# Performance work log

Measured on AMD Instinct MI355X. Metric: run time of the kernel, lower is better.

The kernel has to match this reference:

```python
import jax, jax.numpy as jnp
import numpy as np

N = 4096      # nodes (= attention seq_len)
D = 256       # dim_h
H = 4         # num_heads
HD = D // H   # head dim
E = 131072    # edges (avg degree 32)


def _ln(x, g, b, eps=1e-5):
    mu = jnp.mean(x, -1, keepdims=True)
    var = jnp.var(x, -1, keepdims=True)
    return (x - mu) * jax.lax.rsqrt(var + eps) * g + b


def setup_inputs() -> dict:
    key = jax.random.key(0)
    ks = jax.random.split(key, 10)
    s = 0.02
    nrm = lambda k, shape: jax.random.normal(k, shape, jnp.float32) * s
    return dict(
        x=jax.random.normal(ks[0], (N, D), jnp.float32),
        edge_index=jax.random.randint(ks[1], (2, E), 0, N, dtype=jnp.int32),
        W_gcn=nrm(ks[2], (D, D)), b_gcn=jnp.zeros((D,), jnp.float32),
        w_qkv=nrm(ks[3], (D, 3 * D)), b_qkv=jnp.zeros((3 * D,), jnp.float32),
        w_out=nrm(ks[4], (D, D)), b_out=jnp.zeros((D,), jnp.float32),
        g1l=jnp.ones((D,), jnp.float32), beta1l=jnp.zeros((D,), jnp.float32),
        g1a=jnp.ones((D,), jnp.float32), beta1a=jnp.zeros((D,), jnp.float32),
        W1=nrm(ks[5], (D, 2 * D)), bf1=jnp.zeros((2 * D,), jnp.float32),
        W2=nrm(ks[6], (2 * D, D)), bf2=jnp.zeros((D,), jnp.float32),
        g2=jnp.ones((D,), jnp.float32), beta2=jnp.zeros((D,), jnp.float32),
    )


def reference(x, edge_index, W_gcn, b_gcn, w_qkv, b_qkv, w_out, b_out,
              g1l, beta1l, g1a, beta1a, W1, bf1, W2, bf2, g2, beta2):
    n = x.shape[0]
    # --- GCNConv: sym-normalized aggregation with self loops ---
    loop = jnp.arange(n, dtype=edge_index.dtype)
    src = jnp.concatenate([edge_index[0], loop])
    dst = jnp.concatenate([edge_index[1], loop])
    deg = jax.ops.segment_sum(jnp.ones_like(src, x.dtype), dst, num_segments=n)
    dinv = jax.lax.rsqrt(deg)  # deg >= 1 thanks to self loops
    h = x @ W_gcn                                  # [N, D]
    msg = h[src] * (dinv[src] * dinv[dst])[:, None]  # gather + edge norm
    x_local = jax.ops.segment_sum(msg, dst, num_segments=n) + b_gcn
    x = _ln(x + x_local, g1l, beta1l)
    # --- Multi-head self-attention over all nodes (one sequence) ---
    qkv = x @ w_qkv + b_qkv
    q, k, v = jnp.split(qkv, 3, axis=-1)
    q = q.reshape(n, H, HD)
    k = k.reshape(n, H, HD)
    v = v.reshape(n, H, HD)
    scale = 1.0 / (HD ** 0.5)
    scores = jnp.einsum('nhd,mhd->hnm', q, k) * scale   # [H, N, N]
    attn = jax.nn.softmax(scores, axis=-1)
    x_attn = jnp.einsum('hnm,mhd->nhd', attn, v).reshape(n, D) @ w_out + b_out
    x = _ln(x + x_attn, g1a, beta1a)
    # --- FFN (D -> 2D -> D, ReLU) ---
    x_ffn = jax.nn.relu(x @ W1 + bf1) @ W2 + bf2
    return _ln(x + x_ffn, g2, beta2)
```

## Files before the change

### kernel.cpp

```cpp
#include <hip/hip_runtime.h>

typedef unsigned short u16;
typedef __bf16 bf16x8 __attribute__((ext_vector_type(8)));
typedef float f32x4 __attribute__((ext_vector_type(4)));
typedef float f32x16 __attribute__((ext_vector_type(16)));
typedef unsigned u32x4v __attribute__((ext_vector_type(4)));

__device__ __forceinline__ u16 f2u(float f) {
    unsigned u = __builtin_bit_cast(unsigned, f);
    return (u16)((u + 0x7FFFu + ((u >> 16) & 1u)) >> 16);
}

__device__ __forceinline__ float u2f(u16 h) {
    return __builtin_bit_cast(float, (unsigned)h << 16);
}

__device__ __forceinline__ void glds16(const u16* g, u16* l) {
    __builtin_amdgcn_global_load_lds((const __attribute__((address_space(1))) unsigned int*)g,
                                     (__attribute__((address_space(3))) unsigned int*)l, 16, 0, 0);
}


__global__ __launch_bounds__(256) void prep_k(
    const float* __restrict__ w0, const float* __restrict__ w1, const float* __restrict__ w2,
    const float* __restrict__ w3, const float* __restrict__ w4, const float* __restrict__ x,
    u16* __restrict__ o0, u16* __restrict__ o1, u16* __restrict__ o2,
    u16* __restrict__ o3, u16* __restrict__ o4, u16* __restrict__ xo,
    int* __restrict__ cnt, int xblocks, int nn) {
    int b = blockIdx.x, t = threadIdx.x;
    if (b < 144) {
        const float* in; u16* out; int R, C, tb;
        if (b < 16)       { in = w0; out = o0; R = 256; C = 256; tb = b; }
        else if (b < 64)  { in = w1; out = o1; R = 256; C = 768; tb = b - 16; }
        else if (b < 80)  { in = w2; out = o2; R = 256; C = 256; tb = b - 64; }
        else if (b < 112) { in = w3; out = o3; R = 256; C = 512; tb = b - 80; }
        else              { in = w4; out = o4; R = 512; C = 256; tb = b - 112; }
        int tcols = C >> 6;
        int tr = tb / tcols, tc = tb - tr * tcols;
        __shared__ float T[64][65];
        int i0 = t >> 6, j = t & 63;
#pragma unroll
        for (int p = 0; p < 16; p++) {
            int r = p * 4 + i0;
            T[r][j] = in[(long)(tr * 64 + r) * C + tc * 64 + j];
        }
        __syncthreads();
#pragma unroll
        for (int p = 0; p < 16; p++) {
            int c = p * 4 + i0;
            out[(long)(tc * 64 + c) * R + tr * 64 + j] = f2u(T[j][c]);
        }
    } else if (b < 144 + xblocks) {
        long base = (long)(b - 144) * 4096;
#pragma unroll
        for (int p = 0; p < 4; p++) {
            long idx = base + p * 1024 + t * 4;
            float4 v = *(const float4*)&x[idx];
            unsigned lo = (unsigned)f2u(v.x) | ((unsigned)f2u(v.y) << 16);
            unsigned hi = (unsigned)f2u(v.z) | ((unsigned)f2u(v.w) << 16);
            *(uint2*)&xo[idx] = uint2{lo, hi};
        }
    } else {
        int i = (b - 144 - xblocks) * 256 + t;
        if (i < nn) cnt[i] = 0;
    }
}


__device__ __forceinline__ void block_ln_stats(float v, float& mu, float& rstd) {
    float s1 = v, s2 = v * v;
#pragma unroll
    for (int m = 1; m < 64; m <<= 1) { s1 += __shfl_xor(s1, m, 64); s2 += __shfl_xor(s2, m, 64); }
    __shared__ float r1[4], r2[4];
    int lane = threadIdx.x & 63, w = threadIdx.x >> 6;
    if (lane == 0) { r1[w] = s1; r2[w] = s2; }
    __syncthreads();
    s1 = r1[0] + r1[1] + r1[2] + r1[3];
    s2 = r2[0] + r2[1] + r2[2] + r2[3];
    mu = s1 * (1.0f / 256.0f);
    float var = s2 * (1.0f / 256.0f) - mu * mu;
    rstd = rsqrtf(var + 1e-5f);
}


__global__ __launch_bounds__(256) void gcn_agg_ln_k(
    const u16* __restrict__ h, const float* __restrict__ x,
    const int* __restrict__ srcs, const int* __restrict__ cnt,
    const float* __restrict__ bg,
    const float* __restrict__ g, const float* __restrict__ be,
    float* __restrict__ x1, u16* __restrict__ x1bf) {
    int n = blockIdx.x, d = threadIdx.x;
    int c = cnt[n]; c = c < 128 ? c : 128;
    int st = n << 7;
    float dn = rsqrtf((float)(c + 1));
    float agg = u2f(h[(long)n * 256 + d]) * dn;
    int e = 0;
    for (; e + 4 <= c; e += 4) {
        int s0 = srcs[st + e], s1 = srcs[st + e + 1], s2 = srcs[st + e + 2], s3 = srcs[st + e + 3];
        float a0 = u2f(h[(long)s0 * 256 + d]) * rsqrtf((float)(cnt[s0] + 1));
        float a1 = u2f(h[(long)s1 * 256 + d]) * rsqrtf((float)(cnt[s1] + 1));
        float a2 = u2f(h[(long)s2 * 256 + d]) * rsqrtf((float)(cnt[s2] + 1));
        float a3 = u2f(h[(long)s3 * 256 + d]) * rsqrtf((float)(cnt[s3] + 1));
        agg += (a0 + a1) + (a2 + a3);
    }
    for (; e < c; e++) {
        int s = srcs[st + e];
        agg += u2f(h[(long)s * 256 + d]) * rsqrtf((float)(cnt[s] + 1));
    }
    float v = x[(long)n * 256 + d] + dn * agg + bg[d];
    float mu, rs;
    block_ln_stats(v, mu, rs);
    float y = (v - mu) * rs * g[d] + be[d];
    x1[(long)n * 256 + d] = y;
    x1bf[(long)n * 256 + d] = f2u(y);
}


template <int EPI>
__device__ __forceinline__ void gemm_body(
    int bx, int by,
    const u16* __restrict__ A, const u16* __restrict__ Bt,
    const float* __restrict__ bias, void* __restrict__ outp,
    int M, int N, int K) {
    __shared__ __align__(16) u16 As[64 * 128];
    __shared__ __align__(16) u16 Bs[64 * 128];
    int tid = threadIdx.x;
    int lane = tid & 63, w = tid >> 6;
    int l15 = lane & 15, quad = lane >> 4, l7 = l15 & 7;
    int m0 = bx * 64, n0 = by * 64;
    int wm = (w >> 1) * 32, wn = (w & 1) * 32;
    f32x4 acc[2][2];
#pragma unroll
    for (int i = 0; i < 2; i++)
#pragma unroll
        for (int j = 0; j < 2; j++) acc[i][j] = f32x4{0.f, 0.f, 0.f, 0.f};

    int rA0 = (wm + l15) * 128, rA1 = (wm + 16 + l15) * 128;
    int rB0 = (wn + l15) * 128, rB1 = (wn + 16 + l15) * 128;

    for (int kb = 0; kb < K; kb += 128) {
        if (kb) __syncthreads();
#pragma unroll
        for (int i = 0; i < 4; i++) {
            int s = i * 256 + tid;
            int j = s >> 4, dch = s & 15;
            int c = dch ^ (j & 7);
            glds16(A + (long)(m0 + j) * K + kb + c * 8, &As[s * 8]);
            glds16(Bt + (long)(n0 + j) * K + kb + c * 8, &Bs[s * 8]);
        }
        __syncthreads();
#pragma unroll
        for (int step = 0; step < 4; step++) {
            int d8 = (((step << 2) + quad) ^ l7) << 3;
            bf16x8 af0 = *(const bf16x8*)&As[rA0 + d8];
            bf16x8 af1 = *(const bf16x8*)&As[rA1 + d8];
            bf16x8 bf0 = *(const bf16x8*)&Bs[rB0 + d8];
            bf16x8 bf1 = *(const bf16x8*)&Bs[rB1 + d8];
            acc[0][0] = __builtin_amdgcn_mfma_f32_16x16x32_bf16(af0, bf0, acc[0][0], 0, 0, 0);
            acc[0][1] = __builtin_amdgcn_mfma_f32_16x16x32_bf16(af0, bf1, acc[0][1], 0, 0, 0);
            acc[1][0] = __builtin_amdgcn_mfma_f32_16x16x32_bf16(af1, bf0, acc[1][0], 0, 0, 0);
            acc[1][1] = __builtin_amdgcn_mfma_f32_16x16x32_bf16(af1, bf1, acc[1][1], 0, 0, 0);
        }
    }

#pragma unroll
    for (int nf = 0; nf < 2; nf++) {
        int col = n0 + wn + nf * 16 + l15;
        float bv = bias ? bias[col] : 0.0f;
#pragma unroll
        for (int mf = 0; mf < 2; mf++) {
#pragma unroll
            for (int r = 0; r < 4; r++) {
                int row = m0 + wm + mf * 16 + quad * 4 + r;
                float v = acc[mf][nf][r] + bv;
                if (EPI == 1) {
                    u16* q = (u16*)outp;
                    u16* kk = q + (long)M * 256;
                    u16* vt = kk + (long)M * 256;
                    if (col < 256) {
                        q[(((col >> 6) * (long)M) + row) * 64 + (col & 63)] = f2u(v * 0.180336884f);
                    } else if (col < 512) {
                        int c = col - 256;
                        kk[(((c >> 6) * (long)M) + row) * 64 + (c & 63)] = f2u(v);
                    } else {
                        int c = col - 512;
                        vt[((c >> 6) * 64 + (c & 63)) * (long)M + row] = f2u(v);
                    }
                } else {
                    ((u16*)outp)[(long)row * N + col] = f2u(v);
                }
            }
        }
    }
}

template <int EPI>
__global__ __launch_bounds__(256) void gemm_k(
    const u16* __restrict__ A, const u16* __restrict__ Bt,
    const float* __restrict__ bias, void* __restrict__ outp,
    int M, int N, int K) {
    gemm_body<EPI>(blockIdx.x, blockIdx.y, A, Bt, bias, outp, M, N, K);
}


template <int WRITE_BF>
__global__ __launch_bounds__(512) void gemm_ln_k(
    const u16* __restrict__ A, const u16* __restrict__ Bt, const float* __restrict__ bias,
    const float* __restrict__ res, const float* __restrict__ g, const float* __restrict__ be,
    float* __restrict__ outf, u16* __restrict__ outbf, int M, int K) {
    __shared__ __align__(16) u16 As[16 * 64];
    __shared__ __align__(16) u16 Bs[256 * 64];
    __shared__ float red[2][8][16];
    int tid = threadIdx.x;
    int lane = tid & 63, w = tid >> 6;
    int l15 = lane & 15, quad = lane >> 4, l7 = l15 & 7;
    int m0 = blockIdx.x * 16;
    f32x4 acc[2];
#pragma unroll
    for (int i = 0; i < 2; i++) acc[i] = f32x4{0.f, 0.f, 0.f, 0.f};

    int jA = tid >> 3, dA = tid & 7, cA = dA ^ (jA & 7);
    const u16* agp = A + (long)(m0 + jA) * K + cA * 8;

    for (int kb = 0; kb < K; kb += 64) {
        if (kb) __syncthreads();
        if (tid < 128) glds16(agp + kb, &As[tid * 8]);
#pragma unroll
        for (int i = 0; i < 4; i++) {
            int s = i * 512 + tid;
            int jb = s >> 3, db = s & 7, cb = db ^ (jb & 7);
            glds16(Bt + (long)jb * K + kb + cb * 8, &Bs[s * 8]);
        }
        __syncthreads();
#pragma unroll
        for (int step = 0; step < 2; step++) {
            int d8 = (((step << 2) + quad) ^ l7) << 3;
            bf16x8 af = *(const bf16x8*)&As[l15 * 64 + d8];
#pragma unroll
            for (int nf = 0; nf < 2; nf++) {
                int rb = w * 32 + nf * 16 + l15;
                bf16x8 bfr = *(const bf16x8*)&Bs[rb * 64 + d8];
                acc[nf] = __builtin_amdgcn_mfma_f32_16x16x32_bf16(af, bfr, acc[nf], 0, 0, 0);
            }
        }
    }

    float vv[2][4];
    float p1[4] = {0.f, 0.f, 0.f, 0.f}, p2[4] = {0.f, 0.f, 0.f, 0.f};
#pragma unroll
    for (int nf = 0; nf < 2; nf++) {
        int col = w * 32 + nf * 16 + l15;
        float bv = bias[col];
#pragma unroll
        for (int r = 0; r < 4; r++) {
            int row = m0 + quad * 4 + r;
            float v = acc[nf][r] + bv + res[(long)row * 256 + col];
            vv[nf][r] = v;
            p1[r] += v; p2[r] += v * v;
        }
    }
#pragma unroll
    for (int m = 1; m < 16; m <<= 1) {
#pragma unroll
        for (int r = 0; r < 4; r++) {
            p1[r] += __shfl_xor(p1[r], m, 64);
            p2[r] += __shfl_xor(p2[r], m, 64);
        }
    }
    if (l15 == 0) {
#pragma unroll
        for (int r = 0; r < 4; r++) { red[0][w][quad * 4 + r] = p1[r]; red[1][w][quad * 4 + r] = p2[r]; }
    }
    __syncthreads();
    float mu[4], rs[4];
#pragma unroll
    for (int r = 0; r < 4; r++) {
        int rr = quad * 4 + r;
        float s1 = 0.f, s2 = 0.f;
#pragma unroll
        for (int ww = 0; ww < 8; ww++) { s1 += red[0][ww][rr]; s2 += red[1][ww][rr]; }
        mu[r] = s1 * (1.0f / 256.0f);
        float var = s2 * (1.0f / 256.0f) - mu[r] * mu[r];
        rs[r] = rsqrtf(var + 1e-5f);
    }
#pragma unroll
    for (int nf = 0; nf < 2; nf++) {
        int col = w * 32 + nf * 16 + l15;
        float gg = g[col], bb = be[col];
#pragma unroll
        for (int r = 0; r < 4; r++) {
            int row = m0 + quad * 4 + r;
            float y = (vv[nf][r] - mu[r]) * rs[r] * gg + bb;
            outf[(long)row * 256 + col] = y;
            if (WRITE_BF) outbf[(long)row * 256 + col] = f2u(y);
        }
    }
}


__global__ __launch_bounds__(512) void ffn_fused_k(
    const u16* __restrict__ A, const u16* __restrict__ W1t, const float* __restrict__ b1,
    const u16* __restrict__ W2t, const float* __restrict__ b2v,
    const float* __restrict__ res, const float* __restrict__ g, const float* __restrict__ be,
    float* __restrict__ outf, int M) {
    __shared__ __align__(16) u16 As[16 * 64];
    __shared__ __align__(16) u16 Bs[256 * 64];
    __shared__ __align__(16) u16 Hs[16 * 512];
    __shared__ float red[2][8][16];
    int tid = threadIdx.x;
    int lane = tid & 63, w = tid >> 6;
    int l15 = lane & 15, quad = lane >> 4, l7 = l15 & 7;
    int m0 = blockIdx.x * 16;

    int jA = tid >> 3, dA = tid & 7, cA = dA ^ (jA & 7);
    const u16* agp = A + (long)(m0 + jA) * 256 + cA * 8;

#pragma unroll
    for (int hf = 0; hf < 2; hf++) {
        f32x4 acc[2];
#pragma unroll
        for (int i = 0; i < 2; i++) acc[i] = f32x4{0.f, 0.f, 0.f, 0.f};
        for (int kb = 0; kb < 256; kb += 64) {
            if (hf | kb) __syncthreads();
            if (tid < 128) glds16(agp + kb, &As[tid * 8]);
#pragma unroll
            for (int i = 0; i < 4; i++) {
                int s = i * 512 + tid;
                int jb = s >> 3, db = s & 7, cb = db ^ (jb & 7);
                glds16(W1t + (long)(hf * 256 + jb) * 256 + kb + cb * 8, &Bs[s * 8]);
            }
            __syncthreads();
#pragma unroll
            for (int step = 0; step < 2; step++) {
                int d8 = (((step << 2) + quad) ^ l7) << 3;
                bf16x8 af = *(const bf16x8*)&As[l15 * 64 + d8];
#pragma unroll
                for (int nf = 0; nf < 2; nf++) {
                    int rb = w * 32 + nf * 16 + l15;
                    bf16x8 bfr = *(const bf16x8*)&Bs[rb * 64 + d8];
                    acc[nf] = __builtin_amdgcn_mfma_f32_16x16x32_bf16(af, bfr, acc[nf], 0, 0, 0);
                }
            }
        }
#pragma unroll
        for (int nf = 0; nf < 2; nf++) {
            int col = hf * 256 + w * 32 + nf * 16 + l15;
            float bv = b1[col];
            int g8 = col >> 3, e = col & 7;
#pragma unroll
            for (int r = 0; r < 4; r++) {
                int row = quad * 4 + r;
                float v = acc[nf][r] + bv;
                int slot = (g8 & ~7) | ((g8 & 7) ^ (row & 7));
                Hs[row * 512 + slot * 8 + e] = f2u(v > 0.f ? v : 0.f);
            }
        }
    }

    f32x4 acc[2];
#pragma unroll
    for (int i = 0; i < 2; i++) acc[i] = f32x4{0.f, 0.f, 0.f, 0.f};
    for (int kb = 0; kb < 512; kb += 64) {
        __syncthreads();
#pragma unroll
        for (int i = 0; i < 4; i++) {
            int s = i * 512 + tid;
            int jb = s >> 3, db = s & 7, cb = db ^ (jb & 7);
            glds16(W2t + (long)jb * 512 + kb + cb * 8, &Bs[s * 8]);
        }
        __syncthreads();
#pragma unroll
        for (int step = 0; step < 2; step++) {
            int d8 = (((step << 2) + quad) ^ l7) << 3;
            bf16x8 af = *(const bf16x8*)&Hs[l15 * 512 + kb + d8];
#pragma unroll
            for (int nf = 0; nf < 2; nf++) {
                int rb = w * 32 + nf * 16 + l15;
                bf16x8 bfr = *(const bf16x8*)&Bs[rb * 64 + d8];
                acc[nf] = __builtin_amdgcn_mfma_f32_16x16x32_bf16(af, bfr, acc[nf], 0, 0, 0);
            }
        }
    }

    float vv[2][4];
    float p1[4] = {0.f, 0.f, 0.f, 0.f}, p2[4] = {0.f, 0.f, 0.f, 0.f};
#pragma unroll
    for (int nf = 0; nf < 2; nf++) {
        int col = w * 32 + nf * 16 + l15;
        float bv = b2v[col];
#pragma unroll
        for (int r = 0; r < 4; r++) {
            int row = m0 + quad * 4 + r;
            float v = acc[nf][r] + bv + res[(long)row * 256 + col];
            vv[nf][r] = v;
            p1[r] += v; p2[r] += v * v;
        }
    }
#pragma unroll
    for (int m = 1; m < 16; m <<= 1) {
#pragma unroll
        for (int r = 0; r < 4; r++) {
            p1[r] += __shfl_xor(p1[r], m, 64);
            p2[r] += __shfl_xor(p2[r], m, 64);
        }
    }
    if (l15 == 0) {
#pragma unroll
        for (int r = 0; r < 4; r++) { red[0][w][quad * 4 + r] = p1[r]; red[1][w][quad * 4 + r] = p2[r]; }
    }
    __syncthreads();
    float mu[4], rs[4];
#pragma unroll
    for (int r = 0; r < 4; r++) {
        int rr = quad * 4 + r;
        float s1 = 0.f, s2 = 0.f;
#pragma unroll
        for (int ww = 0; ww < 8; ww++) { s1 += red[0][ww][rr]; s2 += red[1][ww][rr]; }
        mu[r] = s1 * (1.0f / 256.0f);
        float var = s2 * (1.0f / 256.0f) - mu[r] * mu[r];
        rs[r] = rsqrtf(var + 1e-5f);
    }
#pragma unroll
    for (int nf = 0; nf < 2; nf++) {
        int col = w * 32 + nf * 16 + l15;
        float gg = g[col], bb = be[col];
#pragma unroll
        for (int r = 0; r < 4; r++) {
            int row = m0 + quad * 4 + r;
            outf[(long)row * 256 + col] = (vv[nf][r] - mu[r]) * rs[r] * gg + bb;
        }
    }
}


__global__ __launch_bounds__(256) void front_k(
    const int* __restrict__ ei, int E, int* __restrict__ cnt, int* __restrict__ srcs,
    const u16* __restrict__ A, const u16* __restrict__ Bt, void* __restrict__ outp,
    int M, int N, int K, int SB) {
    int b = blockIdx.x;
    if (b < SB) {
        int e = b * 256 + threadIdx.x;
        if (e < E) {
            int s = ei[e], d = ei[E + e];
            int p = atomicAdd(&cnt[d], 1);
            if (p < 128) srcs[(d << 7) + p] = s;
        }
    } else {
        int id = b - SB;
        gemm_body<3>(id & 63, id >> 6, A, Bt, nullptr, outp, M, N, K);
    }
}


__global__ __launch_bounds__(256) void attn_k(const u16* __restrict__ qg, const u16* __restrict__ kg,
                                              const u16* __restrict__ vtg, u16* __restrict__ po,
                                              float* __restrict__ pl, int N, int S) {
    int tid = threadIdx.x;
    int w = tid >> 6, lane = tid & 63;
    int l31 = lane & 31, h = lane >> 5, xr = l31 & 7;
    int qb = blockIdx.x, hh = blockIdx.y, sp = blockIdx.z;
    int q0w = qb * 128 + w * 32;
    int kbeg = sp * (N / S);
    int nit = (N / S) / 64;
    const u16* qh = qg + (long)hh * N * 64;
    const u16* kh = kg + (long)hh * N * 64;
    const u16* vh = vtg + (long)hh * 64 * N;

    __shared__ __align__(16) u16 KV[2][2][4096];

    int s0 = tid, j0 = s0 >> 3, c0s = ((s0 & 7) ^ (j0 & 7)) * 8;
    int s1 = tid + 256, j1 = s1 >> 3, c1s = ((s1 & 7) ^ (j1 & 7)) * 8;
    const u16* kp0 = kh + (long)(kbeg + j0) * 64 + c0s;
    const u16* kp1 = kh + (long)(kbeg + j1) * 64 + c1s;
    const u16* vp0 = vh + (long)j0 * N + kbeg + c0s;
    const u16* vp1 = vh + (long)j1 * N + kbeg + c1s;
    u16* lk0[2] = {&KV[0][0][s0 * 8], &KV[1][0][s0 * 8]};
    u16* lk1[2] = {&KV[0][0][s1 * 8], &KV[1][0][s1 * 8]};
    u16* lv0[2] = {&KV[0][1][s0 * 8], &KV[1][1][s0 * 8]};
    u16* lv1[2] = {&KV[0][1][s1 * 8], &KV[1][1][s1 * 8]};

    bf16x8 qf[4];
#pragma unroll
    for (int stp = 0; stp < 4; stp++)
        qf[stp] = *(const bf16x8*)(qh + (long)(q0w + l31) * 64 + stp * 16 + h * 8);

    f32x16 o0{}, o1{};
    float ll = 0.f;

    glds16(kp0, lk0[0]); glds16(kp1, lk1[0]);
    glds16(vp0, lv0[0]); glds16(vp1, lv1[0]);
    kp0 += 4096; kp1 += 4096; vp0 += 64; vp1 += 64;

    for (int it = 0; it < nit; it++) {
        __syncthreads();
        if (it + 1 < nit) {
            int nb = (it + 1) & 1;
            glds16(kp0, lk0[nb]); glds16(kp1, lk1[nb]);
            glds16(vp0, lv0[nb]); glds16(vp1, lv1[nb]);
            kp0 += 4096; kp1 += 4096; vp0 += 64; vp1 += 64;
        }
        const u16* Kc = &KV[it & 1][0][0];
        const u16* Vc = &KV[it & 1][1][0];

        f32x16 sA{}, sB{};
#pragma unroll
        for (int stp = 0; stp < 4; stp++) {
            int cc = (((stp << 1) + h) ^ xr) * 8;
            bf16x8 kfa = *(const bf16x8*)&Kc[l31 * 64 + cc];
            bf16x8 kfb = *(const bf16x8*)&Kc[(32 + l31) * 64 + cc];
            sA = __builtin_amdgcn_mfma_f32_32x32x16_bf16(kfa, qf[stp], sA, 0, 0, 0);
            sB = __builtin_amdgcn_mfma_f32_32x32x16_bf16(kfb, qf[stp], sB, 0, 0, 0);
        }

#pragma unroll
        for (int kt = 0; kt < 2; kt++) {
            f32x16 s = kt ? sB : sA;
            unsigned wr[8];
#pragma unroll
            for (int i = 0; i < 8; i++) {
                unsigned ua = (unsigned)((int)(s[2 * i] * 8388608.0f) + 1064992209);
                unsigned ub = (unsigned)((int)(s[2 * i + 1] * 8388608.0f) + 1064992209);
                ll += __builtin_bit_cast(float, ua & 0xffff0000u);
                ll += __builtin_bit_cast(float, ub & 0xffff0000u);
                wr[i] = __builtin_amdgcn_perm(ub, ua, 0x07060302u);
            }
            asm("v_permlane32_swap_b32 %0, %1" : "+v"(wr[2]), "+v"(wr[0]));
            asm("v_permlane32_swap_b32 %0, %1" : "+v"(wr[3]), "+v"(wr[1]));
            asm("v_permlane32_swap_b32 %0, %1" : "+v"(wr[6]), "+v"(wr[4]));
            asm("v_permlane32_swap_b32 %0, %1" : "+v"(wr[7]), "+v"(wr[5]));
            u32x4v t0 = {wr[0], wr[1], wr[2], wr[3]};
            u32x4v t1 = {wr[4], wr[5], wr[6], wr[7]};
            bf16x8 f0 = __builtin_bit_cast(bf16x8, t0);
            bf16x8 f1 = __builtin_bit_cast(bf16x8, t1);

#pragma unroll
            for (int dt = 0; dt < 2; dt++) {
                int rowb = (dt * 32 + l31) * 64;
                bf16x8 v0 = *(const bf16x8*)&Vc[rowb + (((kt << 2) + h) ^ xr) * 8];
                bf16x8 v1 = *(const bf16x8*)&Vc[rowb + (((kt << 2) + 2 + h) ^ xr) * 8];
                if (dt == 0) {
                    o0 = __builtin_amdgcn_mfma_f32_32x32x16_bf16(f0, v0, o0, 0, 0, 0);
                    o0 = __builtin_amdgcn_mfma_f32_32x32x16_bf16(f1, v1, o0, 0, 0, 0);
                } else {
                    o1 = __builtin_amdgcn_mfma_f32_32x32x16_bf16(f0, v0, o1, 0, 0, 0);
                    o1 = __builtin_amdgcn_mfma_f32_32x32x16_bf16(f1, v1, o1, 0, 0, 0);
                }
            }
        }
    }

    ll += __shfl_xor(ll, 32, 64);
    long pbase = ((long)(sp * 4 + hh)) * N;
#pragma unroll
    for (int dt = 0; dt < 2; dt++)
#pragma unroll
        for (int r = 0; r < 16; r++) {
            int qrow = q0w + (r & 3) + ((r >> 2) << 3) + (h << 2);
            float val = dt ? o1[r] : o0[r];
            po[(pbase + qrow) * 64 + dt * 32 + l31] = f2u(val);
        }
    if (lane < 32) pl[pbase + q0w + lane] = ll;
}

__global__ __launch_bounds__(256) void attn_comb_k(const u16* __restrict__ po, const float* __restrict__ pl,
                                                   u16* __restrict__ xo, int N, int S) {
    int n = blockIdx.x, c = threadIdx.x;
    int hh = c >> 6, d = c & 63;
    float osum = 0.f, lsum = 0.f;
    for (int s = 0; s < S; s++) {
        osum += u2f(po[(((long)(s * 4 + hh)) * N + n) * 64 + d]);
        lsum += pl[((long)(s * 4 + hh)) * N + n];
    }
    xo[(long)n * 256 + c] = f2u(osum / lsum);
}


extern "C" void kernel_launch(void* const* d_in, const int* in_sizes, int n_in,
                              void* d_out, int out_size, void* d_ws, size_t ws_size,
                              hipStream_t stream) {
    const float* x    = (const float*)d_in[0];
    const int*   ei   = (const int*)d_in[1];
    const float* Wg   = (const float*)d_in[2];
    const float* bg   = (const float*)d_in[3];
    const float* Wqkv = (const float*)d_in[4];
    const float* bqkv = (const float*)d_in[5];
    const float* Wo   = (const float*)d_in[6];
    const float* bo   = (const float*)d_in[7];
    const float* g1l  = (const float*)d_in[8];
    const float* b1l  = (const float*)d_in[9];
    const float* g1a  = (const float*)d_in[10];
    const float* b1a  = (const float*)d_in[11];
    const float* W1   = (const float*)d_in[12];
    const float* bf1  = (const float*)d_in[13];
    const float* W2   = (const float*)d_in[14];
    const float* bf2  = (const float*)d_in[15];
    const float* g2   = (const float*)d_in[16];
    const float* b2   = (const float*)d_in[17];
    float* out = (float*)d_out;

    int N = in_sizes[0] / 256;
    int E = in_sizes[1] / 2;
    const int S = 8;

    char* p = (char*)d_ws;
    auto alloc = [&](size_t bytes) { void* r = (void*)p; p += (bytes + 255) & ~(size_t)255; return r; };
    u16*   wg_t   = (u16*)alloc((size_t)256 * 256 * 2);
    u16*   wqkv_t = (u16*)alloc((size_t)256 * 768 * 2);
    u16*   wo_t   = (u16*)alloc((size_t)256 * 256 * 2);
    u16*   w1_t   = (u16*)alloc((size_t)512 * 256 * 2);
    u16*   w2_t   = (u16*)alloc((size_t)256 * 512 * 2);
    u16*   xbf    = (u16*)alloc((size_t)N * 256 * 2);
    u16*   h      = (u16*)alloc((size_t)N * 256 * 2);
    int*   cnt    = (int*)alloc((size_t)N * 4);
    int*   srcs   = (int*)alloc((size_t)N * 128 * 4);
    float* x1     = (float*)alloc((size_t)N * 256 * 4);
    u16*   x1bf   = (u16*)alloc((size_t)N * 256 * 2);
    u16*   qkv    = (u16*)alloc((size_t)3 * N * 256 * 2);
    u16*   xattn  = (u16*)alloc((size_t)N * 256 * 2);
    float* x2     = (float*)alloc((size_t)N * 256 * 4);
    u16*   x2bf   = (u16*)alloc((size_t)N * 256 * 2);
    u16*   po     = (u16*)alloc((size_t)S * 4 * N * 64 * 2);
    float* pl     = (float*)alloc((size_t)S * 4 * N * 4);

    dim3 b256(256);

    int xblocks = (N * 256) / 4096;
    int cblocks = (N + 255) / 256;
    prep_k<<<144 + xblocks + cblocks, b256, 0, stream>>>(Wg, Wqkv, Wo, W1, W2, x,
                                                         wg_t, wqkv_t, wo_t, w1_t, w2_t, xbf,
                                                         cnt, xblocks, N);

    int SB = (E + 255) / 256;
    front_k<<<SB + (N / 64) * 4, b256, 0, stream>>>(ei, E, cnt, srcs, xbf, wg_t, h, N, 256, 256, SB);

    gcn_agg_ln_k<<<N, b256, 0, stream>>>(h, x, srcs, cnt, bg, g1l, b1l, x1, x1bf);

    gemm_k<1><<<dim3(N / 64, 12), b256, 0, stream>>>(x1bf, wqkv_t, bqkv, qkv, N, 768, 256);

    attn_k<<<dim3(N / 128, 4, S), b256, 0, stream>>>(qkv, qkv + (size_t)N * 256, qkv + (size_t)2 * N * 256,
                                                     po, pl, N, S);
    attn_comb_k<<<N, b256, 0, stream>>>(po, pl, xattn, N, S);

    gemm_ln_k<1><<<N / 16, dim3(512), 0, stream>>>(xattn, wo_t, bo, x1, g1a, b1a, x2, x2bf, N, 256);

    ffn_fused_k<<<N / 16, dim3(512), 0, stream>>>(x2bf, w1_t, bf1, w2_t, bf2, x2, g2, b2, out, N);
}
```

Baseline: 189.0 us.

## Accumulate split-KV attention partials with atomics and fuse combine into out-proj GEMM

Attention splits now atomicAdd their fp32 partial outputs and row sums into one zeroed N×256 buffer instead of writing per-split bf16 partials. The separate combine kernel is removed, and the output-projection GEMM+LN kernel does the normalisation (po/pl) while staging A into LDS. This cuts a launch and the S-fold partial-buffer traffic. In exchange it adds zeroing work in prep, fp32 atomic contention across the 8 splits, and nondeterministic summation order.

```diff
diff --git a/kernel.cpp b/kernel.cpp
--- a/kernel.cpp
+++ b/kernel.cpp
@@ -26,7 +26,7 @@
     const float* __restrict__ w3, const float* __restrict__ w4, const float* __restrict__ x,
     u16* __restrict__ o0, u16* __restrict__ o1, u16* __restrict__ o2,
     u16* __restrict__ o3, u16* __restrict__ o4, u16* __restrict__ xo,
-    int* __restrict__ cnt, int xblocks, int nn) {
+    float* __restrict__ pz, int* __restrict__ cnt, int xblocks, int zblocks, int nn) {
     int b = blockIdx.x, t = threadIdx.x;
     if (b < 144) {
         const float* in; u16* out; int R, C, tb;
@@ -60,8 +60,15 @@
             unsigned hi = (unsigned)f2u(v.z) | ((unsigned)f2u(v.w) << 16);
             *(uint2*)&xo[idx] = uint2{lo, hi};
         }
+    } else if (b < 144 + xblocks + zblocks) {
+        long base = (long)(b - 144 - xblocks) * 4096;
+#pragma unroll
+        for (int p = 0; p < 4; p++) {
+            long idx = base + p * 1024 + t * 4;
+            *(float4*)&pz[idx] = float4{0.f, 0.f, 0.f, 0.f};
+        }
     } else {
-        int i = (b - 144 - xblocks) * 256 + t;
+        int i = (b - 144 - xblocks - zblocks) * 256 + t;
         if (i < nn) cnt[i] = 0;
     }
 }
@@ -203,39 +210,55 @@
 }
 
 
-template <int WRITE_BF>
-__global__ __launch_bounds__(512) void gemm_ln_k(
-    const u16* __restrict__ A, const u16* __restrict__ Bt, const float* __restrict__ bias,
+__global__ __launch_bounds__(512) void comb_gemm_ln_k(
+    const float* __restrict__ po, const float* __restrict__ pl,
+    const u16* __restrict__ Bt, const float* __restrict__ bias,
     const float* __restrict__ res, const float* __restrict__ g, const float* __restrict__ be,
-    float* __restrict__ outf, u16* __restrict__ outbf, int M, int K) {
-    __shared__ __align__(16) u16 As[16 * 64];
+    float* __restrict__ outf, u16* __restrict__ outbf, int M) {
+    const int K = 256;
+    __shared__ __align__(16) u16 As16[16 * 256];
     __shared__ __align__(16) u16 Bs[256 * 64];
     __shared__ float red[2][8][16];
     int tid = threadIdx.x;
     int lane = tid & 63, w = tid >> 6;
     int l15 = lane & 15, quad = lane >> 4, l7 = l15 & 7;
     int m0 = blockIdx.x * 16;
+
+#pragma unroll
+    for (int i = 0; i < 4; i++) {
+        int s = i * 512 + tid;
+        int jb = s >> 3, db = s & 7, cb = db ^ (jb & 7);
+        glds16(Bt + (long)jb * K + cb * 8, &Bs[s * 8]);
+    }
+#pragma unroll
+    for (int i = 0; i < 8; i++) {
+        int idx = i * 512 + tid;
+        int r = idx >> 8, c = idx & 255;
+        float v = po[(long)(m0 + r) * 256 + c] / pl[(m0 + r) * 4 + (c >> 6)];
+        int g8 = c >> 3, e = c & 7;
+        int slot = (g8 & ~7) | ((g8 & 7) ^ (r & 7));
+        As16[r * 256 + slot * 8 + e] = f2u(v);
+    }
+
     f32x4 acc[2];
-#pragma unroll
-    for (int i = 0; i < 2; i++) acc[i] = f32x4{0.f, 0.f, 0.f, 0.f};
-
-    int jA = tid >> 3, dA = tid & 7, cA = dA ^ (jA & 7);
-    const u16* agp = A + (long)(m0 + jA) * K + cA * 8;
+    acc[0] = f32x4{0.f, 0.f, 0.f, 0.f};
+    acc[1] = f32x4{0.f, 0.f, 0.f, 0.f};
 
     for (int kb = 0; kb < K; kb += 64) {
-        if (kb) __syncthreads();
-        if (tid < 128) glds16(agp + kb, &As[tid * 8]);
-#pragma unroll
-        for (int i = 0; i < 4; i++) {
-            int s = i * 512 + tid;
-            int jb = s >> 3, db = s & 7, cb = db ^ (jb & 7);
-            glds16(Bt + (long)jb * K + kb + cb * 8, &Bs[s * 8]);
+        if (kb) {
+            __syncthreads();
+#pragma unroll
+            for (int i = 0; i < 4; i++) {
+                int s = i * 512 + tid;
+                int jb = s >> 3, db = s & 7, cb = db ^ (jb & 7);
+                glds16(Bt + (long)jb * K + kb + cb * 8, &Bs[s * 8]);
+            }
         }
         __syncthreads();
 #pragma unroll
         for (int step = 0; step < 2; step++) {
             int d8 = (((step << 2) + quad) ^ l7) << 3;
-            bf16x8 af = *(const bf16x8*)&As[l15 * 64 + d8];
+            bf16x8 af = *(const bf16x8*)&As16[l15 * 256 + kb + d8];
 #pragma unroll
             for (int nf = 0; nf < 2; nf++) {
                 int rb = w * 32 + nf * 16 + l15;
@@ -292,7 +315,7 @@
             int row = m0 + quad * 4 + r;
             float y = (vv[nf][r] - mu[r]) * rs[r] * gg + bb;
             outf[(long)row * 256 + col] = y;
-            if (WRITE_BF) outbf[(long)row * 256 + col] = f2u(y);
+            outbf[(long)row * 256 + col] = f2u(y);
         }
     }
 }
@@ -453,7 +476,7 @@
 
 
 __global__ __launch_bounds__(256) void attn_k(const u16* __restrict__ qg, const u16* __restrict__ kg,
-                                              const u16* __restrict__ vtg, u16* __restrict__ po,
+                                              const u16* __restrict__ vtg, float* __restrict__ po,
                                               float* __restrict__ pl, int N, int S) {
     int tid = threadIdx.x;
     int w = tid >> 6, lane = tid & 63;
@@ -550,28 +573,15 @@
     }
 
     ll += __shfl_xor(ll, 32, 64);
-    long pbase = ((long)(sp * 4 + hh)) * N;
 #pragma unroll
     for (int dt = 0; dt < 2; dt++)
 #pragma unroll
         for (int r = 0; r < 16; r++) {
             int qrow = q0w + (r & 3) + ((r >> 2) << 3) + (h << 2);
             float val = dt ? o1[r] : o0[r];
-            po[(pbase + qrow) * 64 + dt * 32 + l31] = f2u(val);
-        }
-    if (lane < 32) pl[pbase + q0w + lane] = ll;
-}
-
-__global__ __launch_bounds__(256) void attn_comb_k(const u16* __restrict__ po, const float* __restrict__ pl,
-                                                   u16* __restrict__ xo, int N, int S) {
-    int n = blockIdx.x, c = threadIdx.x;
-    int hh = c >> 6, d = c & 63;
-    float osum = 0.f, lsum = 0.f;
-    for (int s = 0; s < S; s++) {
-        osum += u2f(po[(((long)(s * 4 + hh)) * N + n) * 64 + d]);
-        lsum += pl[((long)(s * 4 + hh)) * N + n];
-    }
-    xo[(long)n * 256 + c] = f2u(osum / lsum);
+            atomicAdd(&po[(long)qrow * 256 + hh * 64 + dt * 32 + l31], val);
+        }
+    if (h == 0) atomicAdd(&pl[(q0w + l31) * 4 + hh], ll);
 }
 
 
@@ -616,19 +626,20 @@
     float* x1     = (float*)alloc((size_t)N * 256 * 4);
     u16*   x1bf   = (u16*)alloc((size_t)N * 256 * 2);
     u16*   qkv    = (u16*)alloc((size_t)3 * N * 256 * 2);
-    u16*   xattn  = (u16*)alloc((size_t)N * 256 * 2);
     float* x2     = (float*)alloc((size_t)N * 256 * 4);
     u16*   x2bf   = (u16*)alloc((size_t)N * 256 * 2);
-    u16*   po     = (u16*)alloc((size_t)S * 4 * N * 64 * 2);
-    float* pl     = (float*)alloc((size_t)S * 4 * N * 4);
+    float* popl   = (float*)alloc((size_t)N * 260 * 4);
+    float* po     = popl;
+    float* pl     = popl + (size_t)N * 256;
 
     dim3 b256(256);
 
     int xblocks = (N * 256) / 4096;
+    int zblocks = (N * 260) / 4096;
     int cblocks = (N + 255) / 256;
-    prep_k<<<144 + xblocks + cblocks, b256, 0, stream>>>(Wg, Wqkv, Wo, W1, W2, x,
-                                                         wg_t, wqkv_t, wo_t, w1_t, w2_t, xbf,
-                                                         cnt, xblocks, N);
+    prep_k<<<144 + xblocks + zblocks + cblocks, b256, 0, stream>>>(
+        Wg, Wqkv, Wo, W1, W2, x, wg_t, wqkv_t, wo_t, w1_t, w2_t, xbf,
+        popl, cnt, xblocks, zblocks, N);
 
     int SB = (E + 255) / 256;
     front_k<<<SB + (N / 64) * 4, b256, 0, stream>>>(ei, E, cnt, srcs, xbf, wg_t, h, N, 256, 256, SB);
@@ -639,9 +650,8 @@
 
     attn_k<<<dim3(N / 128, 4, S), b256, 0, stream>>>(qkv, qkv + (size_t)N * 256, qkv + (size_t)2 * N * 256,
                                                      po, pl, N, S);
-    attn_comb_k<<<N, b256, 0, stream>>>(po, pl, xattn, N, S);
-
-    gemm_ln_k<1><<<N / 16, dim3(512), 0, stream>>>(xattn, wo_t, bo, x1, g1a, b1a, x2, x2bf, N, 256);
+
+    comb_gemm_ln_k<<<N / 16, dim3(512), 0, stream>>>(po, pl, wo_t, bo, x1, g1a, b1a, x2, x2bf, N);
 
     ffn_fused_k<<<N / 16, dim3(512), 0, stream>>>(x2bf, w1_t, bf1, w2_t, bf2, x2, g2, b2, out, N);
 }
```

Result: slower. 195.1 us (+3.2%).
